# Kernel optimization log

Measured on AMD Instinct MI355X. Metric: run time of the kernel, lower is better.

## Reference

```python
import jax, jax.numpy as jnp
import numpy as np


def setup_inputs() -> dict:
    key = jax.random.key(0)
    x = jax.random.normal(key, (4096, 16384), dtype=jnp.float32)
    return {"x": x, "k": 128}


def reference(x, k):
    # top-k along last dim, ReLU the values, scatter back into zeros
    values, indices = jax.lax.top_k(x, k)            # [N, k]
    values = jax.nn.relu(values)
    rows = jnp.arange(x.shape[0])[:, None]            # [N, 1] broadcast over k
    result = jnp.zeros_like(x).at[rows, indices].set(values)
    return result
```

## Files before the change

kernel.cpp:

```cpp
#include <hip/hip_runtime.h>

#define T 512
#define EPT 32
#define ROWLEN 16384
#define BINS1 4096
#define NW (T / 64)
#define EQCAP 512

__device__ __forceinline__ unsigned f2ord(float f) {
    unsigned b = __float_as_uint(f);
    return b ^ ((b & 0x80000000u) ? 0xFFFFFFFFu : 0x80000000u);
}
__device__ __forceinline__ float ord2f(unsigned u) {
    unsigned b = (u & 0x80000000u) ? (u ^ 0x80000000u) : ~u;
    return __uint_as_float(b);
}

__device__ __forceinline__ void select_bin(const int* hist, int BINS, int k,
                                           int* waveSum, int* sh_b, int* sh_k) {
    const int tid  = threadIdx.x;
    const int lane = tid & 63;
    const int w    = tid >> 6;

    int bpt = (BINS + T - 1) / T;
    int lo  = tid * bpt; if (lo > BINS) lo = BINS;
    int hi  = lo + bpt;  if (hi > BINS) hi = BINS;

    int p = 0;
    for (int d = lo; d < hi; ++d) p += hist[d];

    int v = p;
    #pragma unroll
    for (int off = 1; off < 64; off <<= 1) {
        int t2 = __shfl_down(v, off);
        if (lane + off < 64) v += t2;
    }
    if (lane == 0) waveSum[w] = v;
    __syncthreads();

    int carry = 0;
    for (int w2 = w + 1; w2 < NW; ++w2) carry += waveSum[w2];

    int P  = v + carry;
    int Pn = P - p;
    if (P >= k && Pn < k) {
        int running = Pn;
        for (int d = hi - 1; d >= lo; --d) {
            running += hist[d];
            if (running >= k) {
                *sh_b = d;
                *sh_k = k - (running - hist[d]);
                break;
            }
        }
    }
    __syncthreads();
}

__global__ __launch_bounds__(T, 4) void topk_relu_scatter(
        const float* __restrict__ x, const int* __restrict__ kptr,
        float* __restrict__ out) {
    __shared__ int hist[BINS1];
    __shared__ int waveSum[NW];
    __shared__ int sh_b, sh_k;
    __shared__ int sh_idxcut;
    __shared__ int eqCount;
    __shared__ int eqIdx[EQCAP];

    const int tid = threadIdx.x;
    const int row = blockIdx.x;
    const float4* xrow = (const float4*)(x + (size_t)row * ROWLEN);
    float4*       orow = (float4*)(out + (size_t)row * ROWLEN);

    unsigned u[EPT];
    #pragma unroll
    for (int j4 = 0; j4 < EPT / 4; ++j4) {
        float4 v = xrow[tid + T * j4];
        u[4 * j4 + 0] = f2ord(v.x);
        u[4 * j4 + 1] = f2ord(v.y);
        u[4 * j4 + 2] = f2ord(v.z);
        u[4 * j4 + 3] = f2ord(v.w);
    }

    int k = *kptr;

    for (int i = tid; i < BINS1; i += T) hist[i] = 0;
    __syncthreads();
    #pragma unroll
    for (int j = 0; j < EPT; ++j) atomicAdd(&hist[u[j] >> 20], 1);
    __syncthreads();
    select_bin(hist, 4096, k, waveSum, &sh_b, &sh_k);
    unsigned b1 = (unsigned)sh_b; k = sh_k;

    for (int i = tid; i < BINS1; i += T) hist[i] = 0;
    __syncthreads();
    #pragma unroll
    for (int j = 0; j < EPT; ++j)
        if ((u[j] >> 20) == b1) atomicAdd(&hist[(u[j] >> 8) & 0xFFFu], 1);
    __syncthreads();
    select_bin(hist, 4096, k, waveSum, &sh_b, &sh_k);
    unsigned pref2 = (b1 << 12) | (unsigned)sh_b; k = sh_k;

    for (int i = tid; i < BINS1; i += T) hist[i] = 0;
    __syncthreads();
    #pragma unroll
    for (int j = 0; j < EPT; ++j)
        if ((u[j] >> 8) == pref2) atomicAdd(&hist[u[j] & 0xFFu], 1);
    __syncthreads();
    select_bin(hist, 256, k, waveSum, &sh_b, &sh_k);
    const unsigned ustar = (pref2 << 8) | (unsigned)sh_b;
    const int t_eq = sh_k;

    if (tid == 0) eqCount = 0;
    __syncthreads();
    #pragma unroll
    for (int j = 0; j < EPT; ++j) {
        if (u[j] == ustar) {
            int pos = atomicAdd(&eqCount, 1);
            if (pos < EQCAP) {
                int idx = 4 * (tid + T * (j >> 2)) + (j & 3);
                eqIdx[pos] = idx;
            }
        }
    }
    __syncthreads();
    if (tid == 0) {
        int m = eqCount; if (m > EQCAP) m = EQCAP;
        int cut;
        if (t_eq >= m) {
            cut = ROWLEN;
        } else {
            cut = -1;
            for (int it = 0; it < t_eq; ++it) {
                int mn = 0x7FFFFFFF, mi = -1;
                for (int i = 0; i < m; ++i)
                    if (eqIdx[i] < mn) { mn = eqIdx[i]; mi = i; }
                cut = mn; eqIdx[mi] = 0x7FFFFFFF;
            }
        }
        sh_idxcut = cut;
    }
    __syncthreads();
    const int idxcut = sh_idxcut;

    #pragma unroll
    for (int j4 = 0; j4 < EPT / 4; ++j4) {
        float4 o;
        float* op = &o.x;
        #pragma unroll
        for (int c = 0; c < 4; ++c) {
            unsigned uu = u[4 * j4 + c];
            int idx = 4 * (tid + T * j4) + c;
            bool sel = (uu > ustar) || (uu == ustar && idx <= idxcut);
            float xv = ord2f(uu);
            op[c] = (sel && xv > 0.0f) ? xv : 0.0f;
        }
        orow[tid + T * j4] = o;
    }
}

extern "C" void kernel_launch(void* const* d_in, const int* in_sizes, int n_in,
                              void* d_out, int out_size, void* d_ws, size_t ws_size,
                              hipStream_t stream) {
    const float* x    = (const float*)d_in[0];
    const int*   kptr = (const int*)d_in[1];
    float*       out  = (float*)d_out;
    int rows = in_sizes[0] / ROWLEN;
    topk_relu_scatter<<<rows, T, 0, stream>>>(x, kptr, out);
}
```

Before: 448.9 us.

## Compact first-pass candidates and refine radix select on compacted list

Doubles the block to 1024 threads with 16 elements each. After the first 12-bit histogram pass, elements in the selected bin are compacted into a shared candidate list, and the remaining two 10-bit passes run over that list instead of all per-thread registers. A full-register fallback handles overflow beyond the list's capacity. The serial single-thread tie resolution is replaced by a block-wide binary search on index. The aim is to cut histogram work and the serial tie loop, at the cost of more barriers and a larger block.

```diff
diff --git a/kernel.cpp b/kernel.cpp
--- a/kernel.cpp
+++ b/kernel.cpp
@@ -1,11 +1,12 @@
 #include <hip/hip_runtime.h>
 
-#define T 512
-#define EPT 32
+#define T 1024
+#define EPT 16
 #define ROWLEN 16384
-#define BINS1 4096
 #define NW (T / 64)
-#define EQCAP 512
+#define B1 4096
+#define B2 1024
+#define CAP 768
 
 __device__ __forceinline__ unsigned f2ord(float f) {
     unsigned b = __float_as_uint(f);
@@ -39,7 +40,8 @@
     __syncthreads();
 
     int carry = 0;
-    for (int w2 = w + 1; w2 < NW; ++w2) carry += waveSum[w2];
+    #pragma unroll
+    for (int w2 = 0; w2 < NW; ++w2) if (w2 > w) carry += waveSum[w2];
 
     int P  = v + carry;
     int Pn = P - p;
@@ -60,12 +62,11 @@
 __global__ __launch_bounds__(T, 4) void topk_relu_scatter(
         const float* __restrict__ x, const int* __restrict__ kptr,
         float* __restrict__ out) {
-    __shared__ int hist[BINS1];
+    __shared__ int hist[B1];
     __shared__ int waveSum[NW];
     __shared__ int sh_b, sh_k;
-    __shared__ int sh_idxcut;
-    __shared__ int eqCount;
-    __shared__ int eqIdx[EQCAP];
+    __shared__ int candCnt, sh_meq, sh_cnt;
+    __shared__ unsigned candU[CAP];
 
     const int tid = threadIdx.x;
     const int row = blockIdx.x;
@@ -84,64 +85,100 @@
 
     int k = *kptr;
 
-    for (int i = tid; i < BINS1; i += T) hist[i] = 0;
+    #pragma unroll
+    for (int i = 0; i < B1 / T; ++i) hist[tid + T * i] = 0;
+    if (tid == 0) candCnt = 0;
     __syncthreads();
     #pragma unroll
     for (int j = 0; j < EPT; ++j) atomicAdd(&hist[u[j] >> 20], 1);
     __syncthreads();
-    select_bin(hist, 4096, k, waveSum, &sh_b, &sh_k);
-    unsigned b1 = (unsigned)sh_b; k = sh_k;
-
-    for (int i = tid; i < BINS1; i += T) hist[i] = 0;
-    __syncthreads();
-    #pragma unroll
-    for (int j = 0; j < EPT; ++j)
-        if ((u[j] >> 20) == b1) atomicAdd(&hist[(u[j] >> 8) & 0xFFFu], 1);
-    __syncthreads();
-    select_bin(hist, 4096, k, waveSum, &sh_b, &sh_k);
-    unsigned pref2 = (b1 << 12) | (unsigned)sh_b; k = sh_k;
-
-    for (int i = tid; i < BINS1; i += T) hist[i] = 0;
-    __syncthreads();
-    #pragma unroll
-    for (int j = 0; j < EPT; ++j)
-        if ((u[j] >> 8) == pref2) atomicAdd(&hist[u[j] & 0xFFu], 1);
-    __syncthreads();
-    select_bin(hist, 256, k, waveSum, &sh_b, &sh_k);
-    const unsigned ustar = (pref2 << 8) | (unsigned)sh_b;
-    const int t_eq = sh_k;
-
-    if (tid == 0) eqCount = 0;
-    __syncthreads();
+    select_bin(hist, B1, k, waveSum, &sh_b, &sh_k);
+    const unsigned b1 = (unsigned)sh_b; k = sh_k;
+
     #pragma unroll
     for (int j = 0; j < EPT; ++j) {
-        if (u[j] == ustar) {
-            int pos = atomicAdd(&eqCount, 1);
-            if (pos < EQCAP) {
+        if ((u[j] >> 20) == b1) {
+            int p = atomicAdd(&candCnt, 1);
+            if (p < CAP) candU[p] = u[j];
+        }
+    }
+    __syncthreads();
+    const int m = candCnt;
+
+    unsigned ustar; int t_eq;
+    if (m <= CAP) {
+        #pragma unroll
+        for (int i = 0; i < B2 / T; ++i) hist[tid + T * i] = 0;
+        __syncthreads();
+        if (tid < m) atomicAdd(&hist[(candU[tid] >> 10) & 0x3FFu], 1);
+        __syncthreads();
+        select_bin(hist, B2, k, waveSum, &sh_b, &sh_k);
+        const unsigned pref22 = (b1 << 10) | (unsigned)sh_b; k = sh_k;
+
+        for (int i = 0; i < B2 / T; ++i) hist[tid + T * i] = 0;
+        __syncthreads();
+        if (tid < m) {
+            unsigned c = candU[tid];
+            if ((c >> 10) == pref22) atomicAdd(&hist[c & 0x3FFu], 1);
+        }
+        __syncthreads();
+        select_bin(hist, B2, k, waveSum, &sh_b, &sh_k);
+        ustar = (pref22 << 10) | (unsigned)sh_b;
+        t_eq  = sh_k;
+    } else {
+        #pragma unroll
+        for (int i = 0; i < B1 / T; ++i) hist[tid + T * i] = 0;
+        __syncthreads();
+        #pragma unroll
+        for (int j = 0; j < EPT; ++j)
+            if ((u[j] >> 20) == b1) atomicAdd(&hist[(u[j] >> 8) & 0xFFFu], 1);
+        __syncthreads();
+        select_bin(hist, B1, k, waveSum, &sh_b, &sh_k);
+        const unsigned pref24 = (b1 << 12) | (unsigned)sh_b; k = sh_k;
+
+        for (int i = tid; i < 256; i += T) hist[i] = 0;
+        __syncthreads();
+        #pragma unroll
+        for (int j = 0; j < EPT; ++j)
+            if ((u[j] >> 8) == pref24) atomicAdd(&hist[u[j] & 0xFFu], 1);
+        __syncthreads();
+        select_bin(hist, 256, k, waveSum, &sh_b, &sh_k);
+        ustar = (pref24 << 8) | (unsigned)sh_b;
+        t_eq  = sh_k;
+    }
+
+    if (tid == 0) sh_meq = 0;
+    __syncthreads();
+    int local = 0;
+    #pragma unroll
+    for (int j = 0; j < EPT; ++j) local += (u[j] == ustar);
+    if (local) atomicAdd(&sh_meq, local);
+    __syncthreads();
+    const int meq = sh_meq;
+
+    int idxcut;
+    if (t_eq >= meq) {
+        idxcut = ROWLEN;
+    } else {
+        int lo = 0, hi = ROWLEN - 1;
+        while (lo < hi) {
+            int mid = (lo + hi) >> 1;
+            if (tid == 0) sh_cnt = 0;
+            __syncthreads();
+            int c2 = 0;
+            #pragma unroll
+            for (int j = 0; j < EPT; ++j) {
                 int idx = 4 * (tid + T * (j >> 2)) + (j & 3);
-                eqIdx[pos] = idx;
+                c2 += (u[j] == ustar && idx <= mid);
             }
-        }
-    }
-    __syncthreads();
-    if (tid == 0) {
-        int m = eqCount; if (m > EQCAP) m = EQCAP;
-        int cut;
-        if (t_eq >= m) {
-            cut = ROWLEN;
-        } else {
-            cut = -1;
-            for (int it = 0; it < t_eq; ++it) {
-                int mn = 0x7FFFFFFF, mi = -1;
-                for (int i = 0; i < m; ++i)
-                    if (eqIdx[i] < mn) { mn = eqIdx[i]; mi = i; }
-                cut = mn; eqIdx[mi] = 0x7FFFFFFF;
-            }
-        }
-        sh_idxcut = cut;
-    }
-    __syncthreads();
-    const int idxcut = sh_idxcut;
+            if (c2) atomicAdd(&sh_cnt, c2);
+            __syncthreads();
+            int cnt = sh_cnt;
+            __syncthreads();
+            if (cnt >= t_eq) hi = mid; else lo = mid + 1;
+        }
+        idxcut = lo;
+    }
 
     #pragma unroll
     for (int j4 = 0; j4 < EPT / 4; ++j4) {
```

New measurement: 477.6 us. 6.4% more time.
